# Kernel tuning notes

Measured on AMD Instinct MI355X. Metric: run time of the kernel, lower is better.

## Reference

```python
import jax, jax.numpy as jnp
import numpy as np
import math

D_MODEL = 1024
NUM_HEADS = 16
D_K = D_MODEL // NUM_HEADS
MAX_SEQ_LEN = 2048
THETA = 10000.0
BATCH = 2
SEQ = 2048


def _rope_tables():
    inv_freq = THETA ** (-jnp.arange(0, D_K, 2, dtype=jnp.float32) / D_K)  # [d_k/2]
    pos = jnp.arange(MAX_SEQ_LEN, dtype=jnp.float32)                      # [max_seq]
    ang = pos[:, None] * inv_freq[None, :]                                # [max_seq, d_k/2]
    return jnp.cos(ang), jnp.sin(ang)


def _apply_rope(x, token_positions, cos_tab, sin_tab):
    # x: [b, h, s, d_k]; token_positions: [b, s]
    cos = cos_tab[token_positions][:, None, :, :]  # [b,1,s,d_k/2]
    sin = sin_tab[token_positions][:, None, :, :]
    xp = x.reshape(*x.shape[:-1], D_K // 2, 2)     # interleaved pairs
    xe, xo = xp[..., 0], xp[..., 1]
    oe = xe * cos - xo * sin
    oo = xe * sin + xo * cos
    return jnp.stack((oe, oo), axis=-1).reshape(x.shape)


def setup_inputs() -> dict:
    key = jax.random.key(0)
    ks = jax.random.split(key, 5)
    std = math.sqrt(2.0 / (D_MODEL + D_MODEL))
    x = jax.random.normal(ks[0], (BATCH, SEQ, D_MODEL), dtype=jnp.float32)
    wq = jax.random.normal(ks[1], (D_MODEL, D_MODEL), dtype=jnp.float32) * std
    wk = jax.random.normal(ks[2], (D_MODEL, D_MODEL), dtype=jnp.float32) * std
    wv = jax.random.normal(ks[3], (D_MODEL, D_MODEL), dtype=jnp.float32) * std
    wo = jax.random.normal(ks[4], (D_MODEL, D_MODEL), dtype=jnp.float32) * std
    token_positions = jnp.broadcast_to(jnp.arange(SEQ, dtype=jnp.int32), (BATCH, SEQ))
    return {"x": x, "wq": wq, "wk": wk, "wv": wv, "wo": wo,
            "token_positions": token_positions}


def reference(x, wq, wk, wv, wo, token_positions):
    b, s, _ = x.shape
    cos_tab, sin_tab = _rope_tables()

    def proj_heads(w):
        y = jnp.einsum('oi,bsi->bso', w, x)  # Linear: w[d_out,d_in]
        return y.reshape(b, s, NUM_HEADS, D_K).transpose(0, 2, 1, 3)  # [b,h,s,d_k]

    q = proj_heads(wq)
    k = proj_heads(wk)
    v = proj_heads(wv)
    q = _apply_rope(q, token_positions, cos_tab, sin_tab)
    k = _apply_rope(k, token_positions, cos_tab, sin_tab)

    scores = jnp.einsum('bhqd,bhkd->bhqk', q, k) / math.sqrt(D_K)
    causal = jnp.tril(jnp.ones((s, s), dtype=bool))
    scores = jnp.where(causal, scores, -jnp.inf)
    attn = jax.nn.softmax(scores, axis=-1)
    out = jnp.einsum('bhqk,bhkd->bhqd', attn, v)
    out = out.transpose(0, 2, 1, 3).reshape(b, s, D_MODEL)
    return jnp.einsum('oi,bsi->bso', wo, out)
```

## Files before the change

kernel.cpp:

```cpp
#include <hip/hip_runtime.h>
#include <cstdint>
#include <cstddef>

#define NH 16
#define DK 64
#define DM 1024
#define SEQL 2048
#define NB 2
#define NR (NB * SEQL)

typedef short bf16x8 __attribute__((ext_vector_type(8)));
typedef float f32x4 __attribute__((ext_vector_type(4)));

static __device__ __forceinline__ float bf2f(short u) {
  union { unsigned int i; float f; } x;
  x.i = ((unsigned int)(unsigned short)u) << 16;
  return x.f;
}
static __device__ __forceinline__ short f2bf(float f) {
  union { unsigned int i; float f; } x;
  x.f = f;
  unsigned int r = x.i + 0x7fffu + ((x.i >> 16) & 1u);
  return (short)(r >> 16);
}
static __device__ __forceinline__ unsigned cvtpk(float a, float b) {
  unsigned r;
  asm("v_cvt_pk_bf16_f32 %0, %1, %2" : "=v"(r) : "v"(a), "v"(b));
  return r;
}

static __device__ __forceinline__ void gload16(const short* g, short* l) {
  __builtin_amdgcn_global_load_lds((const __attribute__((address_space(1))) void*)g,
                                   (__attribute__((address_space(3))) void*)l, 16, 0, 0);
}

__global__ void cvt_all(const float* __restrict__ x, const float* __restrict__ w0,
                        const float* __restrict__ w1, const float* __restrict__ w2,
                        const float* __restrict__ w3, short* __restrict__ xb,
                        short* __restrict__ o0, short* __restrict__ o1,
                        short* __restrict__ o2, short* __restrict__ o3) {
  int y = blockIdx.y;
  const float* in;
  short* out;
  if (y < 4) { in = x + (size_t)y * DM * DM; out = xb + (size_t)y * DM * DM; }
  else if (y == 4) { in = w0; out = o0; }
  else if (y == 5) { in = w1; out = o1; }
  else if (y == 6) { in = w2; out = o2; }
  else { in = w3; out = o3; }
  int i = (blockIdx.x * blockDim.x + threadIdx.x) * 4;
  float4 v = *reinterpret_cast<const float4*>(in + i);
  short4 o;
  o.x = f2bf(v.x); o.y = f2bf(v.y); o.z = f2bf(v.z); o.w = f2bf(v.w);
  *reinterpret_cast<short4*>(out + i) = o;
}

__global__ void rope_table_kernel(float2* __restrict__ tab) {
  int idx = blockIdx.x * blockDim.x + threadIdx.x;
  int pos = idx >> 5, j = idx & 31;
  float freq = powf(10000.0f, -(float)j / 32.0f);
  float ang = (float)pos * freq;
  tab[idx] = make_float2(cosf(ang), sinf(ang));
}

__global__ void rope_apply_kernel(short* __restrict__ Qb, short* __restrict__ Kb,
                                  const int* __restrict__ pos, const float2* __restrict__ tab) {
  short* buf = blockIdx.y ? Kb : Qb;
  const float scale = blockIdx.y ? 1.0f : 0.1803368801f;
  int gid = blockIdx.x * blockDim.x + threadIdx.x;
  int elem = gid * 8;
  int row = elem >> 10, off = elem & 1023;
  int j0 = (off & 63) >> 1;
  short* ptr = buf + (size_t)row * DM + off;
  bf16x8 v = *reinterpret_cast<bf16x8*>(ptr);
  const float2* tp = &tab[pos[row] * 32 + j0];
  bf16x8 o;
#pragma unroll
  for (int q = 0; q < 4; ++q) {
    float2 cs = tp[q];
    float xe = bf2f(v[2 * q]), xo = bf2f(v[2 * q + 1]);
    o[2 * q] = f2bf((xe * cs.x - xo * cs.y) * scale);
    o[2 * q + 1] = f2bf((xe * cs.y + xo * cs.x) * scale);
  }
  *reinterpret_cast<bf16x8*>(ptr) = o;
}

__global__ __launch_bounds__(256) void vt_transpose_kernel(const short* __restrict__ V,
                                                           short* __restrict__ Vt) {
  __shared__ short tile[64][64];
  const int t = threadIdx.x;
  const int bh = blockIdx.y, b = bh >> 4, h = bh & 15;
  const int st = blockIdx.x * 64;
#pragma unroll
  for (int p = 0; p < 2; ++p) {
    int c = p * 256 + t;
    int srow = c >> 3, ch = c & 7;
    int chs = ch ^ ((srow >> 3) & 7);
    *reinterpret_cast<bf16x8*>(&tile[srow][chs * 8]) =
        *reinterpret_cast<const bf16x8*>(&V[(size_t)(b * SEQL + st + srow) * DM + h * 64 + ch * 8]);
  }
  __syncthreads();
#pragma unroll
  for (int p = 0; p < 2; ++p) {
    int c = p * 256 + t;
    int drow = c >> 3, soff = (c & 7) * 8;
    short o[8];
#pragma unroll
    for (int e = 0; e < 8; ++e) {
      int srow = soff + e;
      int col = (((drow >> 3) ^ ((srow >> 3) & 7)) << 3) + (drow & 7);
      o[e] = tile[srow][col];
    }
    *reinterpret_cast<bf16x8*>(&Vt[(size_t)(bh * DK + drow) * SEQL + st + soff]) =
        *reinterpret_cast<bf16x8*>(o);
  }
}

static __device__ __forceinline__ void gemm_core(const short* __restrict__ A,
                                                 const short* __restrict__ B,
                                                 int m0, int n0, int K,
                                                 f32x4 (&acc)[4][4]) {
  __shared__ short As[128][32];
  __shared__ short Bs[128][32];
  const int t = threadIdx.x;
  const int wid = t >> 6, lane = t & 63;
  const int wr = wid >> 1, wc = wid & 1;
  const int lrow = lane & 15, lk = lane >> 4;

#pragma unroll
  for (int i = 0; i < 4; ++i)
#pragma unroll
    for (int j = 0; j < 4; ++j) acc[i][j] = (f32x4){0.f, 0.f, 0.f, 0.f};

  for (int k0 = 0; k0 < K; k0 += 32) {
    __syncthreads();
#pragma unroll
    for (int p = 0; p < 2; ++p) {
      int c = p * 256 + t;
      int row = c >> 2, kc = (c & 3) * 8;
      gload16(&A[(size_t)(m0 + row) * K + k0 + kc], &As[0][0] + (size_t)(p * 256 + wid * 64) * 8);
      gload16(&B[(size_t)(n0 + row) * K + k0 + kc], &Bs[0][0] + (size_t)(p * 256 + wid * 64) * 8);
    }
    __syncthreads();
    bf16x8 af[4], bfr[4];
#pragma unroll
    for (int i = 0; i < 4; ++i) {
      af[i] = *reinterpret_cast<const bf16x8*>(&As[wr * 64 + i * 16 + lrow][lk * 8]);
      bfr[i] = *reinterpret_cast<const bf16x8*>(&Bs[wc * 64 + i * 16 + lrow][lk * 8]);
    }
    __builtin_amdgcn_s_setprio(1);
#pragma unroll
    for (int i = 0; i < 4; ++i)
#pragma unroll
      for (int j = 0; j < 4; ++j)
        acc[i][j] = __builtin_amdgcn_mfma_f32_16x16x32_bf16(af[i], bfr[j], acc[i][j], 0, 0, 0);
    __builtin_amdgcn_s_setprio(0);
  }
}

__global__ __launch_bounds__(256) void qkv_gemm_kernel(
    const short* __restrict__ X, const short* __restrict__ Wq, const short* __restrict__ Wk,
    const short* __restrict__ Wv, short* __restrict__ Qb, short* __restrict__ Kb,
    short* __restrict__ Vb) {
  const int nb = blockIdx.x;
  const short* Bw = (nb < 8) ? Wq : (nb < 16) ? Wk : Wv;
  short* C = (nb < 8) ? Qb : (nb < 16) ? Kb : Vb;
  const int m0 = blockIdx.y * 128, n0 = (nb & 7) * 128;
  f32x4 acc[4][4];
  gemm_core(X, Bw, m0, n0, DM, acc);

  const int t = threadIdx.x;
  const int wid = t >> 6, lane = t & 63;
  const int wr = wid >> 1, wc = wid & 1;
  const int lrow = lane & 15, lk = lane >> 4;
#pragma unroll
  for (int i = 0; i < 4; ++i)
#pragma unroll
    for (int j = 0; j < 4; ++j) {
      int row = m0 + wr * 64 + i * 16 + lk * 4;
      int col = n0 + wc * 64 + j * 16 + lrow;
#pragma unroll
      for (int r = 0; r < 4; ++r) C[(size_t)(row + r) * DM + col] = f2bf(acc[i][j][r]);
    }
}

__global__ __launch_bounds__(256) void out_gemm_kernel(const short* __restrict__ A,
                                                       const short* __restrict__ W,
                                                       float* __restrict__ C) {
  const int m0 = blockIdx.y * 128, n0 = blockIdx.x * 128;
  f32x4 acc[4][4];
  gemm_core(A, W, m0, n0, DM, acc);
  const int t = threadIdx.x;
  const int wid = t >> 6, lane = t & 63;
  const int wr = wid >> 1, wc = wid & 1;
  const int lrow = lane & 15, lk = lane >> 4;
#pragma unroll
  for (int i = 0; i < 4; ++i)
#pragma unroll
    for (int j = 0; j < 4; ++j) {
      int row = m0 + wr * 64 + i * 16 + lk * 4;
      int col = n0 + wc * 64 + j * 16 + lrow;
#pragma unroll
      for (int r = 0; r < 4; ++r) C[(size_t)(row + r) * DM + col] = acc[i][j][r];
    }
}

__global__ __launch_bounds__(512) void attn_kernel(const short* __restrict__ Q,
                                                   const short* __restrict__ K,
                                                   const short* __restrict__ Vt,
                                                   short* __restrict__ O) {
  __shared__ short Ks[64][72];
  __shared__ short Vs[64][72];
  __shared__ short Ps[8][16][72];
  const int t = threadIdx.x;
  const int wid = t >> 6, lane = t & 63;
  const int lrow = lane & 15, lk = lane >> 4;
  const int lin = blockIdx.x;
  const int xcd = lin & 7, idx = lin >> 3;
  const int qt = (idx < 32) ? (15 - (idx >> 2)) : ((idx - 32) >> 2);
  const int bh = xcd * 4 + (idx & 3);
  const int b = bh >> 4, h = bh & 15;
  const size_t base = (size_t)b * SEQL * DM + (size_t)h * DK;
  const size_t vbase = (size_t)bh * DK * SEQL;
  const int kr = t >> 3, ko = (t & 7) * 8;
  const int ktmax = 2 * qt + 1;
  const int qmin = qt * 128 + wid * 16;
  const int dkt = qmin >> 6;

  bf16x8 aq[2];
#pragma unroll
  for (int c = 0; c < 2; ++c)
    aq[c] = *reinterpret_cast<const bf16x8*>(
        &Q[base + (size_t)(qmin + lrow) * DM + c * 32 + lk * 8]);

  bf16x8 vones;
#pragma unroll
  for (int e = 0; e < 8; ++e) vones[e] = (short)0x3F80;

  f32x4 oacc[4];
#pragma unroll
  for (int g = 0; g < 4; ++g) oacc[g] = (f32x4){0.f, 0.f, 0.f, 0.f};
  f32x4 oaccL = (f32x4){0.f, 0.f, 0.f, 0.f};

  {
    bf16x8 k0 = *reinterpret_cast<const bf16x8*>(&K[base + (size_t)kr * DM + ko]);
    bf16x8 v0 = *reinterpret_cast<const bf16x8*>(&Vt[vbase + (size_t)kr * SEQL + ko]);
    *reinterpret_cast<bf16x8*>(&Ks[kr][ko]) = k0;
    *reinterpret_cast<bf16x8*>(&Vs[kr][ko]) = v0;
  }
  bf16x8 kreg, vreg;
  for (int kt = 0; kt <= ktmax; ++kt) {
    __syncthreads();
    if (kt < ktmax) {
      size_t kof = (size_t)(kt + 1) * 64;
      kreg = *reinterpret_cast<const bf16x8*>(&K[base + (kof + kr) * DM + ko]);
      vreg = *reinterpret_cast<const bf16x8*>(&Vt[vbase + (size_t)kr * SEQL + kof + ko]);
    }
    if (kt <= dkt) {
      f32x4 st[4];
      __builtin_amdgcn_s_setprio(1);
#pragma unroll
      for (int g = 0; g < 4; ++g) {
        bf16x8 kf0 = *reinterpret_cast<const bf16x8*>(&Ks[g * 16 + lrow][lk * 8]);
        bf16x8 kf1 = *reinterpret_cast<const bf16x8*>(&Ks[g * 16 + lrow][32 + lk * 8]);
        f32x4 z = (f32x4){0.f, 0.f, 0.f, 0.f};
        z = __builtin_amdgcn_mfma_f32_16x16x32_bf16(kf0, aq[0], z, 0, 0, 0);
        st[g] = __builtin_amdgcn_mfma_f32_16x16x32_bf16(kf1, aq[1], z, 0, 0, 0);
      }
      __builtin_amdgcn_s_setprio(0);
      const int qg = qmin + lrow;
      if (kt == dkt) {
#pragma unroll
        for (int g = 0; g < 4; ++g)
#pragma unroll
          for (int r = 0; r < 4; ++r)
            if (kt * 64 + g * 16 + lk * 4 + r > qg) st[g][r] = -1e30f;
      }
#pragma unroll
      for (int g = 0; g < 4; ++g)
#pragma unroll
        for (int r = 0; r < 4; ++r) st[g][r] = exp2f(st[g][r]);
#pragma unroll
      for (int g = 0; g < 4; ++g) {
        uint2 wv = make_uint2(cvtpk(st[g][0], st[g][1]), cvtpk(st[g][2], st[g][3]));
        *reinterpret_cast<uint2*>(&Ps[wid][lrow][g * 16 + lk * 4]) = wv;
      }
      asm volatile("s_waitcnt lgkmcnt(0)" ::: "memory");
      __builtin_amdgcn_sched_barrier(0);
      bf16x8 pa0 = *reinterpret_cast<const bf16x8*>(&Ps[wid][lrow][lk * 8]);
      bf16x8 pa1 = *reinterpret_cast<const bf16x8*>(&Ps[wid][lrow][32 + lk * 8]);
      __builtin_amdgcn_s_setprio(1);
#pragma unroll
      for (int g = 0; g < 4; ++g) {
        bf16x8 vf0 = *reinterpret_cast<const bf16x8*>(&Vs[g * 16 + lrow][lk * 8]);
        bf16x8 vf1 = *reinterpret_cast<const bf16x8*>(&Vs[g * 16 + lrow][32 + lk * 8]);
        oacc[g] = __builtin_amdgcn_mfma_f32_16x16x32_bf16(pa0, vf0, oacc[g], 0, 0, 0);
        oacc[g] = __builtin_amdgcn_mfma_f32_16x16x32_bf16(pa1, vf1, oacc[g], 0, 0, 0);
      }
      oaccL = __builtin_amdgcn_mfma_f32_16x16x32_bf16(pa0, vones, oaccL, 0, 0, 0);
      oaccL = __builtin_amdgcn_mfma_f32_16x16x32_bf16(pa1, vones, oaccL, 0, 0, 0);
      __builtin_amdgcn_s_setprio(0);
    }
    __syncthreads();
    if (kt < ktmax) {
      *reinterpret_cast<bf16x8*>(&Ks[kr][ko]) = kreg;
      *reinterpret_cast<bf16x8*>(&Vs[kr][ko]) = vreg;
    }
  }
  float lr[4];
#pragma unroll
  for (int r = 0; r < 4; ++r) lr[r] = 1.0f / oaccL[r];
#pragma unroll
  for (int g = 0; g < 4; ++g)
#pragma unroll
    for (int r = 0; r < 4; ++r)
      O[base + (size_t)(qmin + lk * 4 + r) * DM + g * 16 + lrow] = f2bf(oacc[g][r] * lr[r]);
}

extern "C" void kernel_launch(void* const* d_in, const int* in_sizes, int n_in,
                              void* d_out, int out_size, void* d_ws, size_t ws_size,
                              hipStream_t stream) {
  const float* x = (const float*)d_in[0];
  const float* wq = (const float*)d_in[1];
  const float* wk = (const float*)d_in[2];
  const float* wv = (const float*)d_in[3];
  const float* wo = (const float*)d_in[4];
  const int* tpos = (const int*)d_in[5];
  float* out = (float*)d_out;

  char* w = (char*)d_ws;
  short* xb = (short*)w;  w += (size_t)NR * DM * 2;
  short* wqb = (short*)w; w += (size_t)DM * DM * 2;
  short* wkb = (short*)w; w += (size_t)DM * DM * 2;
  short* wvb = (short*)w; w += (size_t)DM * DM * 2;
  short* wob = (short*)w; w += (size_t)DM * DM * 2;
  short* Qb = (short*)w;  w += (size_t)NR * DM * 2;
  short* Kb = (short*)w;  w += (size_t)NR * DM * 2;
  short* Vb = (short*)w;  w += (size_t)NR * DM * 2;
  short* Ob = (short*)w;  w += (size_t)NR * DM * 2;
  float2* tab = (float2*)w;
  short* Vtb = xb;

  rope_table_kernel<<<2048 * 32 / 256, 256, 0, stream>>>(tab);
  cvt_all<<<dim3(DM * DM / 1024, 8), 256, 0, stream>>>(x, wq, wk, wv, wo, xb, wqb, wkb, wvb, wob);
  qkv_gemm_kernel<<<dim3(24, NR / 128), 256, 0, stream>>>(xb, wqb, wkb, wvb, Qb, Kb, Vb);
  rope_apply_kernel<<<dim3(NR * DM / 8 / 256, 2), 256, 0, stream>>>(Qb, Kb, tpos, tab);
  vt_transpose_kernel<<<dim3(SEQL / 64, NB * NH), 256, 0, stream>>>(Vb, Vtb);
  attn_kernel<<<512, 512, 0, stream>>>(Qb, Kb, Vtb, Ob);
  out_gemm_kernel<<<dim3(DM / 128, NR / 128), 256, 0, stream>>>(Ob, wob, out);
}
```

Baseline: 127.5 us.

## Double-buffer attention K/V tiles and remap GEMM blocks for XCD locality

The attention kernel now keeps two LDS buffers for K and V. The next tile is written into the idle buffer while the current one is consumed, which removes one of the two barriers per iteration. The QKV and output GEMMs switch to 1D grids with a custom block-to-tile mapping. In the QKV GEMM each XCD gets a fixed set of weight column tiles, which is meant to improve L2 reuse of the weights. The attention kernel's LDS use roughly doubles for K and V, which may affect occupancy.

```diff
diff --git a/kernel.cpp b/kernel.cpp
--- a/kernel.cpp
+++ b/kernel.cpp
@@ -161,10 +161,13 @@
     const short* __restrict__ X, const short* __restrict__ Wq, const short* __restrict__ Wk,
     const short* __restrict__ Wv, short* __restrict__ Qb, short* __restrict__ Kb,
     short* __restrict__ Vb) {
-  const int nb = blockIdx.x;
+  const int lin = blockIdx.x;
+  const int xcd = lin & 7, i = lin >> 3;
+  const int nb = xcd * 3 + (i % 3);
+  const int my = i / 3;
   const short* Bw = (nb < 8) ? Wq : (nb < 16) ? Wk : Wv;
   short* C = (nb < 8) ? Qb : (nb < 16) ? Kb : Vb;
-  const int m0 = blockIdx.y * 128, n0 = (nb & 7) * 128;
+  const int m0 = my * 128, n0 = (nb & 7) * 128;
   f32x4 acc[4][4];
   gemm_core(X, Bw, m0, n0, DM, acc);
 
@@ -173,20 +176,21 @@
   const int wr = wid >> 1, wc = wid & 1;
   const int lrow = lane & 15, lk = lane >> 4;
 #pragma unroll
-  for (int i = 0; i < 4; ++i)
+  for (int i2 = 0; i2 < 4; ++i2)
 #pragma unroll
     for (int j = 0; j < 4; ++j) {
-      int row = m0 + wr * 64 + i * 16 + lk * 4;
+      int row = m0 + wr * 64 + i2 * 16 + lk * 4;
       int col = n0 + wc * 64 + j * 16 + lrow;
 #pragma unroll
-      for (int r = 0; r < 4; ++r) C[(size_t)(row + r) * DM + col] = f2bf(acc[i][j][r]);
+      for (int r = 0; r < 4; ++r) C[(size_t)(row + r) * DM + col] = f2bf(acc[i2][j][r]);
     }
 }
 
 __global__ __launch_bounds__(256) void out_gemm_kernel(const short* __restrict__ A,
                                                        const short* __restrict__ W,
                                                        float* __restrict__ C) {
-  const int m0 = blockIdx.y * 128, n0 = blockIdx.x * 128;
+  const int lin = blockIdx.x;
+  const int m0 = (lin >> 3) * 128, n0 = (lin & 7) * 128;
   f32x4 acc[4][4];
   gemm_core(A, W, m0, n0, DM, acc);
   const int t = threadIdx.x;
@@ -208,8 +212,8 @@
                                                    const short* __restrict__ K,
                                                    const short* __restrict__ Vt,
                                                    short* __restrict__ O) {
-  __shared__ short Ks[64][72];
-  __shared__ short Vs[64][72];
+  __shared__ short Ks[2][64][72];
+  __shared__ short Vs[2][64][72];
   __shared__ short Ps[8][16][72];
   const int t = threadIdx.x;
   const int wid = t >> 6, lane = t & 63;
@@ -244,12 +248,13 @@
   {
     bf16x8 k0 = *reinterpret_cast<const bf16x8*>(&K[base + (size_t)kr * DM + ko]);
     bf16x8 v0 = *reinterpret_cast<const bf16x8*>(&Vt[vbase + (size_t)kr * SEQL + ko]);
-    *reinterpret_cast<bf16x8*>(&Ks[kr][ko]) = k0;
-    *reinterpret_cast<bf16x8*>(&Vs[kr][ko]) = v0;
-  }
+    *reinterpret_cast<bf16x8*>(&Ks[0][kr][ko]) = k0;
+    *reinterpret_cast<bf16x8*>(&Vs[0][kr][ko]) = v0;
+  }
+  __syncthreads();
+  int cur = 0;
   bf16x8 kreg, vreg;
   for (int kt = 0; kt <= ktmax; ++kt) {
-    __syncthreads();
     if (kt < ktmax) {
       size_t kof = (size_t)(kt + 1) * 64;
       kreg = *reinterpret_cast<const bf16x8*>(&K[base + (kof + kr) * DM + ko]);
@@ -260,8 +265,8 @@
       __builtin_amdgcn_s_setprio(1);
 #pragma unroll
       for (int g = 0; g < 4; ++g) {
-        bf16x8 kf0 = *reinterpret_cast<const bf16x8*>(&Ks[g * 16 + lrow][lk * 8]);
-        bf16x8 kf1 = *reinterpret_cast<const bf16x8*>(&Ks[g * 16 + lrow][32 + lk * 8]);
+        bf16x8 kf0 = *reinterpret_cast<const bf16x8*>(&Ks[cur][g * 16 + lrow][lk * 8]);
+        bf16x8 kf1 = *reinterpret_cast<const bf16x8*>(&Ks[cur][g * 16 + lrow][32 + lk * 8]);
         f32x4 z = (f32x4){0.f, 0.f, 0.f, 0.f};
         z = __builtin_amdgcn_mfma_f32_16x16x32_bf16(kf0, aq[0], z, 0, 0, 0);
         st[g] = __builtin_amdgcn_mfma_f32_16x16x32_bf16(kf1, aq[1], z, 0, 0, 0);
@@ -291,8 +296,8 @@
       __builtin_amdgcn_s_setprio(1);
 #pragma unroll
       for (int g = 0; g < 4; ++g) {
-        bf16x8 vf0 = *reinterpret_cast<const bf16x8*>(&Vs[g * 16 + lrow][lk * 8]);
-        bf16x8 vf1 = *reinterpret_cast<const bf16x8*>(&Vs[g * 16 + lrow][32 + lk * 8]);
+        bf16x8 vf0 = *reinterpret_cast<const bf16x8*>(&Vs[cur][g * 16 + lrow][lk * 8]);
+        bf16x8 vf1 = *reinterpret_cast<const bf16x8*>(&Vs[cur][g * 16 + lrow][32 + lk * 8]);
         oacc[g] = __builtin_amdgcn_mfma_f32_16x16x32_bf16(pa0, vf0, oacc[g], 0, 0, 0);
         oacc[g] = __builtin_amdgcn_mfma_f32_16x16x32_bf16(pa1, vf1, oacc[g], 0, 0, 0);
       }
@@ -300,11 +305,12 @@
       oaccL = __builtin_amdgcn_mfma_f32_16x16x32_bf16(pa1, vones, oaccL, 0, 0, 0);
       __builtin_amdgcn_s_setprio(0);
     }
+    if (kt < ktmax) {
+      *reinterpret_cast<bf16x8*>(&Ks[cur ^ 1][kr][ko]) = kreg;
+      *reinterpret_cast<bf16x8*>(&Vs[cur ^ 1][kr][ko]) = vreg;
+    }
     __syncthreads();
-    if (kt < ktmax) {
-      *reinterpret_cast<bf16x8*>(&Ks[kr][ko]) = kreg;
-      *reinterpret_cast<bf16x8*>(&Vs[kr][ko]) = vreg;
-    }
+    cur ^= 1;
   }
   float lr[4];
 #pragma unroll
@@ -342,9 +348,9 @@
 
   rope_table_kernel<<<2048 * 32 / 256, 256, 0, stream>>>(tab);
   cvt_all<<<dim3(DM * DM / 1024, 8), 256, 0, stream>>>(x, wq, wk, wv, wo, xb, wqb, wkb, wvb, wob);
-  qkv_gemm_kernel<<<dim3(24, NR / 128), 256, 0, stream>>>(xb, wqb, wkb, wvb, Qb, Kb, Vb);
+  qkv_gemm_kernel<<<768, 256, 0, stream>>>(xb, wqb, wkb, wvb, Qb, Kb, Vb);
   rope_apply_kernel<<<dim3(NR * DM / 8 / 256, 2), 256, 0, stream>>>(Qb, Kb, tpos, tab);
   vt_transpose_kernel<<<dim3(SEQL / 64, NB * NH), 256, 0, stream>>>(Vb, Vtb);
   attn_kernel<<<512, 512, 0, stream>>>(Qb, Kb, Vtb, Ob);
-  out_gemm_kernel<<<dim3(DM / 128, NR / 128), 256, 0, stream>>>(Ob, wob, out);
-}
+  out_gemm_kernel<<<256, 256, 0, stream>>>(Ob, wob, out);
+}
```

Result: no change. 127.8 us (+0.2%).
